# Performance work log

Measured on AMD Instinct MI355X. Metric: run time of the kernel, lower is better.

The kernel has to match this reference:

```python
import jax, jax.numpy as jnp
import numpy as np

B = 4096
D = 64  # emb_dim, hardcoded in UserEmb/ItemEmb


def setup_inputs() -> dict:
    key = jax.random.key(0)
    ks = jax.random.split(key, 26)
    n = lambda k, shape, s=1.0: jax.random.normal(k, shape, dtype=jnp.float32) * s
    inp = {
        'user_emb': jax.random.randint(ks[0], (B, 4), 0, 6, dtype=jnp.int32),
        'item_emb': jax.random.randint(ks[1], (B, 10242), 0, 2, dtype=jnp.int32),
        'edge_emb': jnp.zeros((B,), dtype=jnp.int32),  # edges_emb has num_embeddings=1
        # UserEmb params
        'gender_tab': n(ks[2], (98, D)),
        'age_tab': n(ks[3], (7, D)),
        'occ_tab': n(ks[4], (21, D)),
        'area_tab': n(ks[5], (3402, D)),
        'user_W': n(ks[6], (4 * D, D), 0.05),  # stored [in,out]
        'user_b': n(ks[7], (D,), 0.05),
        # ItemEmb params
        'rate_tab': n(ks[8], (6, D)),
        'genre_W': n(ks[9], (25, D), 0.05),
        'director_W': n(ks[10], (2186, D), 0.02),
        'actor_W': n(ks[11], (8030, D), 0.01),
        'item_W': n(ks[12], (4 * D, D), 0.05),
        'item_b': n(ks[13], (D,), 0.05),
        # GLNFeat params (torch: randn * 0.5)
        'edges_tab': n(ks[14], (1, D)),
        'uu_w': n(ks[15], (D,), 0.5),
        'ui_w': n(ks[16], (D,), 0.5),
        'iu_w': n(ks[17], (D,), 0.5),
        'ii_w': n(ks[18], (D,), 0.5),
        'edge_W': n(ks[19], (D, D), 0.5),
        'uu_W1': n(ks[20], (D, D), 0.5),
        'ui_W1': n(ks[21], (D, D), 0.5),
        'iu_W1': n(ks[22], (D, D), 0.5),
        'ii_W1': n(ks[23], (D, D), 0.5),
    }
    return inp


def _lrelu(v):
    return jnp.where(v >= 0, v, 0.01 * v)  # nn.LeakyReLU default slope


def reference(user_emb, item_emb, edge_emb, gender_tab, age_tab, occ_tab, area_tab,
              user_W, user_b, rate_tab, genre_W, director_W, actor_W, item_W, item_b,
              edges_tab, uu_w, ui_w, iu_w, ii_w, edge_W, uu_W1, ui_W1, iu_W1, ii_W1):
    a = 0.12
    b = 0.12
    # UserEmb
    u_cat = jnp.concatenate([gender_tab[user_emb[:, 0]], age_tab[user_emb[:, 1]],
                             occ_tab[user_emb[:, 2]], area_tab[user_emb[:, 3]]], axis=1)
    x = (u_cat @ user_W + user_b) * a  # [B, D]
    # ItemEmb: multi-hot fields projected then mean-normalized by count
    genre = item_emb[:, 1:26].astype(jnp.float32)
    director = item_emb[:, 26:2212].astype(jnp.float32)
    actor = item_emb[:, 2212:10242].astype(jnp.float32)
    ge = (genre @ genre_W) / jnp.sum(genre, 1, keepdims=True)
    de = (director @ director_W) / jnp.sum(director, 1, keepdims=True)
    ae = (actor @ actor_W) / jnp.sum(actor, 1, keepdims=True)
    i_cat = jnp.concatenate([rate_tab[item_emb[:, 0]], ge, de, ae], axis=1)
    y = (i_cat @ item_W + item_b) * a  # [B, D]
    edge = edges_tab[edge_emb] * b  # [B, D]

    def outer_mm(u, v, M):
        # stop_gradient(outer(u, v) @ M) == u[:,None] * (v @ M), avoids [B,B]
        return jax.lax.stop_gradient(u[:, None] * (v @ M))

    xe = x * edge
    ye = y * edge
    x_xx = xe @ uu_w      # [B]
    x_xy_x = xe @ ui_w
    x_xy_y = ye @ ui_w
    t1 = outer_mm(x_xx, x_xx, x)
    t2 = outer_mm(x_xy_x, x_xy_y, y)
    x_buy = (_lrelu(t1 @ uu_W1) + _lrelu(t2 @ ui_W1)) / 2
    y_yy = ye @ ii_w
    y_yx_y = ye @ iu_w
    y_yx_x = xe @ iu_w
    t3 = outer_mm(y_yy, y_yy, y)
    t4 = outer_mm(y_yx_y, y_yx_x, x)
    y_buy = (_lrelu(t3 @ ii_W1) + _lrelu(t4 @ iu_W1)) / 2
    new = _lrelu(edge @ edge_W)
    return ((x_buy + x) / 2, (y_buy + y) / 2, (new + edge) / 2)
```

## Files before the change

### kernel.cpp

```cpp
#include <hip/hip_runtime.h>
#include <cstddef>

constexpr int BATCH = 4096;
constexpr int ITEM_COLS = 10242;

constexpr int R_GENDER = 0;
constexpr int R_AGE    = 98;
constexpr int R_OCC    = 105;
constexpr int R_AREA   = 126;
constexpr int R_RATE   = 3528;
constexpr int R_FU     = 3534;

__device__ const int CUM[10] = {0, 128, 1280, 2432, 3840, 5248, 6656, 8064, 9472, 10880};
__device__ const int DLT[9]  = {0, -104, -168, -224, -296, -368, -432, -504, -576};
__device__ const int LOG[9]  = {1, 130, 1287, 2436, 3846, 5256, 6659, 8069, 9479};
__device__ const int HIG[9]  = {26, 1223, 2380, 3774, 5184, 6595, 7997, 9407, 10818};
constexpr int FB2COLS = 10880;
constexpr int NTILE   = 85;
constexpr int NSLICE  = 15;
__device__ const int TS_[16] = {0, 1, 7, 13, 19, 25, 31, 37, 43, 49, 55, 61, 67, 73, 79, 85};

constexpr int NFUSEA = 884;
constexpr int NFUSET = FB2COLS / 64;
constexpr int NPACK  = 1024;

struct PackTab { unsigned long long vm[NFUSET]; int c0[NFUSET]; };
constexpr PackTab make_packtab() {
    PackTab p{};
    const int CUMc[10] = {0, 128, 1280, 2432, 3840, 5248, 6656, 8064, 9472, 10880};
    const int DLTc[9]  = {0, -104, -168, -224, -296, -368, -432, -504, -576};
    const int LOGc[9]  = {1, 130, 1287, 2436, 3846, 5256, 6659, 8069, 9479};
    const int HIGc[9]  = {26, 1223, 2380, 3774, 5184, 6595, 7997, 9407, 10818};
    for (int wq = 0; wq < NFUSET; ++wq) {
        int g0 = wq * 64;
        int ch = 0;
        while (g0 >= CUMc[ch + 1]) ++ch;
        int lo = LOGc[ch] - g0; lo = lo < 0 ? 0 : lo;
        int hi = HIGc[ch] - g0; hi = hi < 0 ? 0 : (hi > 64 ? 64 : hi);
        unsigned long long hm = (hi >= 64) ? ~0ull : ((1ull << hi) - 1ull);
        unsigned long long lm = (lo <= 0) ? 0ull : ((1ull << lo) - 1ull);
        p.vm[wq] = hm & ~lm;
        p.c0[wq] = g0 + DLTc[ch];
    }
    return p;
}
__device__ constexpr PackTab PT = make_packtab();

constexpr size_t OFF_FU  = 0;
constexpr size_t OFF_NEW = OFF_FU + (size_t)R_FU * 64;
constexpr size_t OFF_FBT = OFF_NEW + 64;
constexpr size_t OFF_MSK = OFF_FBT + (size_t)64 * FB2COLS / 2;
constexpr size_t OFF_X   = OFF_MSK + (size_t)BATCH * (FB2COLS / 64) * 2;
constexpr size_t OFF_Y   = OFF_X + (size_t)BATCH * 64;
constexpr size_t OFF_P   = OFF_Y + (size_t)BATCH * 64;
constexpr size_t OFF_C   = OFF_P + (size_t)NSLICE * BATCH * 64;
constexpr size_t OFF_SP  = OFF_C + (size_t)NSLICE * BATCH;
constexpr size_t OFF_SC  = OFF_SP + 256ull * 256;

typedef __attribute__((ext_vector_type(8))) short bf16x8;
typedef __attribute__((ext_vector_type(4))) float f32x4;
typedef __attribute__((ext_vector_type(4))) unsigned u32x4;

__device__ __forceinline__ float lrelu(float v) { return v >= 0.0f ? v : 0.01f * v; }

__device__ __forceinline__ unsigned bf_rne_pair(float lo, float hi) {
    unsigned ul = __builtin_bit_cast(unsigned, lo);
    unsigned uh = __builtin_bit_cast(unsigned, hi);
    ul += 0x7fffu + ((ul >> 16) & 1u);
    uh += 0x7fffu + ((uh >> 16) & 1u);
    return (ul >> 16) | (uh & 0xffff0000u);
}

__global__ __launch_bounds__(256) void k_fuse(
        const float* __restrict__ gender_tab, const float* __restrict__ age_tab,
        const float* __restrict__ occ_tab, const float* __restrict__ area_tab,
        const float* __restrict__ user_W, const float* __restrict__ rate_tab,
        const float* __restrict__ item_W, const float* __restrict__ edges_tab,
        const float* __restrict__ edge_W, const float* __restrict__ genre_W,
        const float* __restrict__ director_W, const float* __restrict__ actor_W,
        const int* __restrict__ item,
        float* __restrict__ Fu, float* __restrict__ NEWt, short* __restrict__ B2s,
        unsigned long long* __restrict__ M64) {
    const int t = threadIdx.x;
    const int blk = blockIdx.x;

    if (blk >= NFUSEA + NFUSET) {
        const int w = __builtin_amdgcn_readfirstlane(t >> 6);
        const int lane = t & 63;
        const int m = (blk - (NFUSEA + NFUSET)) * 4 + w;
        const int* row = item + (size_t)m * ITEM_COLS;
        unsigned long long* dst = M64 + (size_t)m * (FB2COLS / 64);
#pragma unroll 2
        for (int wq = 0; wq < FB2COLS / 64; ++wq) {
            int c = PT.c0[wq] + lane;
            c = c > (ITEM_COLS - 1) ? (ITEM_COLS - 1) : c;
            unsigned long long b = __ballot(row[c] != 0) & PT.vm[wq];
            if (lane == 0) dst[wq] = b;
        }
        return;
    }

    const int n = t & 63;
    const int rb = __builtin_amdgcn_readfirstlane(t >> 6);
    __shared__ float T[64 * 65];

    if (blk < NFUSEA) {
        int r = blk * 4 + rb;
        if (r > R_FU) return;
        if (r == R_FU) {
            float acc = 0.0f;
#pragma unroll
            for (int k = 0; k < 64; ++k)
                acc = fmaf(edges_tab[k] * 0.12f, edge_W[k * 64 + n], acc);
            NEWt[n] = lrelu(acc);
            return;
        }
        const float* src;
        const float* W;
        if (r < R_AGE)       { src = gender_tab + (size_t)r * 64;            W = user_W;            }
        else if (r < R_OCC)  { src = age_tab    + (size_t)(r - R_AGE) * 64;  W = user_W + 64 * 64;  }
        else if (r < R_AREA) { src = occ_tab    + (size_t)(r - R_OCC) * 64;  W = user_W + 128 * 64; }
        else if (r < R_RATE) { src = area_tab   + (size_t)(r - R_AREA) * 64; W = user_W + 192 * 64; }
        else                 { src = rate_tab   + (size_t)(r - R_RATE) * 64; W = item_W;            }
        float acc = 0.0f;
#pragma unroll
        for (int k = 0; k < 64; ++k)
            acc = fmaf(src[k], W[k * 64 + n], acc);
        Fu[(size_t)r * 64 + n] = acc;
        return;
    }

    const int g0 = (blk - NFUSEA) * 64;
    int ch = 0;
    while (g0 >= CUM[ch + 1]) ++ch;
    const int lo = LOG[ch], hi = HIG[ch], dl = DLT[ch];

    for (int rl = 0; rl < 16; ++rl) {
        int r = rl * 4 + rb;
        int g = g0 + r;
        float acc = 0.0f;
        if (g >= lo && g < hi) {
            int c = g + dl;
            const float* src;
            const float* W;
            if (c < 26)        { src = genre_W    + (size_t)(c - 1) * 64;    W = item_W + 64 * 64;  }
            else if (c < 2212) { src = director_W + (size_t)(c - 26) * 64;   W = item_W + 128 * 64; }
            else               { src = actor_W    + (size_t)(c - 2212) * 64; W = item_W + 192 * 64; }
#pragma unroll
            for (int k = 0; k < 64; ++k)
                acc = fmaf(src[k], W[k * 64 + n], acc);
        }
        T[r * 65 + n] = acc;
    }
    __syncthreads();
    int n2 = t >> 2, sg = t & 3;
    unsigned dw[8];
#pragma unroll
    for (int d = 0; d < 8; ++d)
        dw[d] = bf_rne_pair(T[(sg * 16 + 2 * d) * 65 + n2], T[(sg * 16 + 2 * d + 1) * 65 + n2]);
    const int kt = g0 >> 7;
    const int kl = (g0 & 127) + sg * 16;
    const int ks = kl >> 5;
    const int qa = (kl >> 3) & 3;
    const int s = n2 >> 4, r16b = n2 & 15;
    const size_t slot0 = (size_t)kt * 1024 + ks * 256 + s * 64 + qa * 16 + r16b;
    *(uint4*)(B2s + slot0 * 8)        = make_uint4(dw[0], dw[1], dw[2], dw[3]);
    *(uint4*)(B2s + (slot0 + 16) * 8) = make_uint4(dw[4], dw[5], dw[6], dw[7]);
}

__global__ __launch_bounds__(256) void k_item(const unsigned long long* __restrict__ M64,
                                              const short* __restrict__ B2s,
                                              float* __restrict__ P, float* __restrict__ C) {
    const int slc = blockIdx.y;
    const int kt0 = TS_[slc], kt1 = TS_[slc + 1];
    const int m0 = blockIdx.x * 64;
    const int t = threadIdx.x;
    const int lane = t & 63;
    const int w = __builtin_amdgcn_readfirstlane(t >> 6);
    const int q = lane >> 4, r16 = lane & 15;
    const int m = m0 + w * 16 + r16;

    f32x4 acc[5];
#pragma unroll
    for (int s = 0; s < 5; ++s) acc[s] = (f32x4){0.f, 0.f, 0.f, 0.f};

    const short o = (r16 == 0) ? (short)0x3f80 : (short)0;
    const bf16x8 ones = {o, o, o, o, o, o, o, o};

    const u32x4* mrow = (const u32x4*)(M64 + (size_t)m * (FB2COLS / 64));
    const bf16x8* b2 = (const bf16x8*)B2s;

    for (int kt = kt0; kt < kt1; ++kt) {
        u32x4 mv = mrow[kt];
        const bf16x8* bp = b2 + (size_t)kt * 1024 + lane;
#pragma unroll
        for (int ks = 0; ks < 4; ++ks) {
            unsigned by = (mv[ks] >> (q * 8)) & 0xffu;
            u32x4 ev;
#pragma unroll
            for (int p2 = 0; p2 < 4; ++p2)
                ev[p2] = (((by >> (2 * p2)) & 1u) ? 0x3f80u : 0u)
                       | (((by >> (2 * p2 + 1)) & 1u) ? 0x3f800000u : 0u);
            bf16x8 a = __builtin_bit_cast(bf16x8, ev);
#pragma unroll
            for (int s = 0; s < 4; ++s) {
                bf16x8 b = bp[ks * 256 + s * 64];
                acc[s] = __builtin_amdgcn_mfma_f32_16x16x32_bf16(a, b, acc[s], 0, 0, 0);
            }
            acc[4] = __builtin_amdgcn_mfma_f32_16x16x32_bf16(a, ones, acc[4], 0, 0, 0);
        }
    }
    const size_t pb = (size_t)slc * BATCH + m0 + w * 16 + q * 4;
#pragma unroll
    for (int reg = 0; reg < 4; ++reg) {
        float* pr = P + (pb + reg) * 64 + r16;
        pr[0] = acc[0][reg];
        pr[16] = acc[1][reg];
        pr[32] = acc[2][reg];
        pr[48] = acc[3][reg];
    }
    if (r16 == 0) {
#pragma unroll
        for (int reg = 0; reg < 4; ++reg)
            C[(size_t)slc * BATCH + m0 + w * 16 + q * 4 + reg] = acc[4][reg];
    }
}

__device__ __forceinline__ float wred(float v) {
#pragma unroll
    for (int m = 1; m < 64; m <<= 1) v += __shfl_xor(v, m, 64);
    return v;
}

__global__ __launch_bounds__(256) void k_mid(const int* __restrict__ item, const int* __restrict__ edge_emb,
                                             const int* __restrict__ user_emb,
                                             const float* __restrict__ Fu, const float* __restrict__ user_b,
                                             const float* __restrict__ P, const float* __restrict__ C,
                                             const float* __restrict__ item_b, const float* __restrict__ edges_tab,
                                             const float* __restrict__ uu_w, const float* __restrict__ ui_w,
                                             const float* __restrict__ iu_w, const float* __restrict__ ii_w,
                                             float* __restrict__ X, float* __restrict__ Y,
                                             float* __restrict__ SC, float* __restrict__ SP) {
    const int t = threadIdx.x;
    const int n = t & 63;
    const int wv = __builtin_amdgcn_readfirstlane(t >> 6);
    const float uuw = uu_w[n], uiw = ui_w[n], iuw = iu_w[n], iiw = ii_w[n];
    const float ib = item_b[n], ub = user_b[n];
    const size_t cs = (size_t)BATCH * 64;
    float s1 = 0.0f, s2 = 0.0f, s3 = 0.0f, s4 = 0.0f;

    for (int i = 0; i < 4; ++i) {
        int b = blockIdx.x * 16 + wv * 4 + i;
        const int* ue = user_emb + (size_t)b * 4;
        float x = (Fu[(size_t)(R_GENDER + ue[0]) * 64 + n]
                 + Fu[(size_t)(R_AGE    + ue[1]) * 64 + n]
                 + Fu[(size_t)(R_OCC    + ue[2]) * 64 + n]
                 + Fu[(size_t)(R_AREA   + ue[3]) * 64 + n] + ub) * 0.12f;
        X[(size_t)b * 64 + n] = x;
        int ri = item[(size_t)b * ITEM_COLS];
        size_t base = (size_t)b * 64 + n;
        float sg = P[base];
        float cg = C[b];
        float sd = 0.0f, cd = 0.0f, sa = 0.0f, ca = 0.0f;
#pragma unroll
        for (int s5 = 1; s5 < 4; ++s5) { sd += P[base + s5 * cs]; cd += C[s5 * BATCH + b]; }
#pragma unroll
        for (int s5 = 4; s5 < NSLICE; ++s5) { sa += P[base + s5 * cs]; ca += C[s5 * BATCH + b]; }
        float y = (Fu[(size_t)(R_RATE + ri) * 64 + n] + sg / cg + sd / cd + sa / ca + ib) * 0.12f;
        Y[(size_t)b * 64 + n] = y;
        float e = edges_tab[(size_t)edge_emb[b] * 64 + n] * 0.12f;
        float xe = x * e, ye = y * e;
        float r1 = wred(xe * uuw);
        float r2 = wred(xe * uiw);
        float r3 = wred(xe * iuw);
        float r4 = wred(ye * uiw);
        float r5 = wred(ye * iiw);
        float r6 = wred(ye * iuw);
        if (n == 0) {
            SC[b] = r1; SC[BATCH + b] = r2; SC[2 * BATCH + b] = r5; SC[3 * BATCH + b] = r6;
        }
        s1 = fmaf(r1, x, s1);
        s2 = fmaf(r4, y, s2);
        s3 = fmaf(r5, y, s3);
        s4 = fmaf(r3, x, s4);
    }
    __shared__ float sp[4][4][64];
    sp[wv][0][n] = s1; sp[wv][1][n] = s2; sp[wv][2][n] = s3; sp[wv][3][n] = s4;
    __syncthreads();
    int i2 = t >> 6;
    float v = sp[0][i2][n] + sp[1][i2][n] + sp[2][i2][n] + sp[3][i2][n];
    SP[(size_t)blockIdx.x * 256 + t] = v;
}

__global__ __launch_bounds__(256) void k_out(const float* __restrict__ X, const float* __restrict__ Y,
                                             const float* __restrict__ SC, const float* __restrict__ SP,
                                             const float* __restrict__ NEWt, const float* __restrict__ edges_tab,
                                             const int* __restrict__ edge_emb,
                                             const float* __restrict__ uu_W1, const float* __restrict__ ui_W1,
                                             const float* __restrict__ iu_W1, const float* __restrict__ ii_W1,
                                             float* __restrict__ out) {
    const int t = threadIdx.x;
    const int i = t >> 6, n = t & 63;
    float s = 0.0f;
    for (int wb = 0; wb < 256; ++wb) s += SP[(size_t)wb * 256 + t];
    __shared__ float sl2[4][64];
    sl2[i][n] = s;
    __syncthreads();
    const float* W1 = (i == 0) ? uu_W1 : (i == 1) ? ui_W1 : (i == 2) ? ii_W1 : iu_W1;
    float p = 0.0f;
#pragma unroll
    for (int k = 0; k < 64; ++k) p = fmaf(sl2[i][k], W1[k * 64 + n], p);
    __shared__ float pbs[4][64];
    pbs[i][n] = p;
    __syncthreads();
    const float p1 = pbs[0][n], p2 = pbs[1][n], p3 = pbs[2][n], p4 = pbs[3][n];
    const float nw = NEWt[n];
#pragma unroll
    for (int j = 0; j < 8; ++j) {
        int b = blockIdx.x * 32 + j * 4 + i;
        float xx = SC[b], xyx = SC[BATCH + b], yy = SC[2 * BATCH + b], yxy = SC[3 * BATCH + b];
        float x = X[(size_t)b * 64 + n], y = Y[(size_t)b * 64 + n];
        float o1 = ((lrelu(xx * p1) + lrelu(xyx * p2)) * 0.5f + x) * 0.5f;
        float o2 = ((lrelu(yy * p3) + lrelu(yxy * p4)) * 0.5f + y) * 0.5f;
        float e = edges_tab[(size_t)edge_emb[b] * 64 + n] * 0.12f;
        float o3 = (nw + e) * 0.5f;
        out[(size_t)b * 64 + n] = o1;
        out[((size_t)BATCH + b) * 64 + n] = o2;
        out[((size_t)2 * BATCH + b) * 64 + n] = o3;
    }
}

extern "C" void kernel_launch(void* const* d_in, const int* in_sizes, int n_in,
                              void* d_out, int out_size, void* d_ws, size_t ws_size,
                              hipStream_t stream) {
    (void)in_sizes; (void)n_in; (void)out_size; (void)ws_size;
    const int*   user_emb   = (const int*)  d_in[0];
    const int*   item_emb   = (const int*)  d_in[1];
    const int*   edge_emb   = (const int*)  d_in[2];
    const float* gender_tab = (const float*)d_in[3];
    const float* age_tab    = (const float*)d_in[4];
    const float* occ_tab    = (const float*)d_in[5];
    const float* area_tab   = (const float*)d_in[6];
    const float* user_W     = (const float*)d_in[7];
    const float* user_b     = (const float*)d_in[8];
    const float* rate_tab   = (const float*)d_in[9];
    const float* genre_W    = (const float*)d_in[10];
    const float* director_W = (const float*)d_in[11];
    const float* actor_W    = (const float*)d_in[12];
    const float* item_W     = (const float*)d_in[13];
    const float* item_b     = (const float*)d_in[14];
    const float* edges_tab  = (const float*)d_in[15];
    const float* uu_w       = (const float*)d_in[16];
    const float* ui_w       = (const float*)d_in[17];
    const float* iu_w       = (const float*)d_in[18];
    const float* ii_w       = (const float*)d_in[19];
    const float* edge_W     = (const float*)d_in[20];
    const float* uu_W1      = (const float*)d_in[21];
    const float* ui_W1      = (const float*)d_in[22];
    const float* iu_W1      = (const float*)d_in[23];
    const float* ii_W1      = (const float*)d_in[24];

    float* ws   = (float*)d_ws;
    float* Fu   = ws + OFF_FU;
    float* NEWt = ws + OFF_NEW;
    short* B2s  = (short*)(ws + OFF_FBT);
    unsigned long long* M64 = (unsigned long long*)(ws + OFF_MSK);
    float* X    = ws + OFF_X;
    float* Y    = ws + OFF_Y;
    float* P    = ws + OFF_P;
    float* C    = ws + OFF_C;
    float* SP   = ws + OFF_SP;
    float* SC   = ws + OFF_SC;
    float* out  = (float*)d_out;

    hipLaunchKernelGGL(k_fuse, dim3(NFUSEA + NFUSET + NPACK), dim3(256), 0, stream,
                       gender_tab, age_tab, occ_tab, area_tab, user_W, rate_tab,
                       item_W, edges_tab, edge_W, genre_W, director_W, actor_W,
                       item_emb, Fu, NEWt, B2s, M64);
    hipLaunchKernelGGL(k_item, dim3(BATCH / 64, NSLICE), dim3(256), 0, stream, M64, B2s, P, C);
    hipLaunchKernelGGL(k_mid, dim3(BATCH / 16), dim3(256), 0, stream,
                       item_emb, edge_emb, user_emb, Fu, user_b, P, C, item_b, edges_tab,
                       uu_w, ui_w, iu_w, ii_w, X, Y, SC, SP);
    hipLaunchKernelGGL(k_out, dim3(BATCH / 32), dim3(256), 0, stream,
                       X, Y, SC, SP, NEWt, edges_tab, edge_emb,
                       uu_W1, ui_W1, iu_W1, ii_W1, out);
}
```

Baseline: 387.2 us.

## Read item multi-hot directly in GEMM kernel, drop bitmask packing pass

Removes the packing stage that ballots the int32 item matrix into 64-bit masks, and instead has the item GEMM kernel read the raw int32 rows and build bf16 one/zero A-fragments on the fly. Full tiles use vectorized int2 loads, and tiles that straddle field boundaries use bounds-checked scalar loads. This eliminates one full read of the ~168MB item matrix plus the mask write/read. The cost is that each GEMM thread now loads 32 bytes per k-step with strided row access instead of 4 bytes of mask, which may make the GEMM more memory-bound.

```diff
diff --git a/kernel.cpp b/kernel.cpp
--- a/kernel.cpp
+++ b/kernel.cpp
@@ -16,41 +16,26 @@
 __device__ const int LOG[9]  = {1, 130, 1287, 2436, 3846, 5256, 6659, 8069, 9479};
 __device__ const int HIG[9]  = {26, 1223, 2380, 3774, 5184, 6595, 7997, 9407, 10818};
 constexpr int FB2COLS = 10880;
-constexpr int NTILE   = 85;
 constexpr int NSLICE  = 15;
 __device__ const int TS_[16] = {0, 1, 7, 13, 19, 25, 31, 37, 43, 49, 55, 61, 67, 73, 79, 85};
+__device__ const int TCH[85] = {
+    0,
+    1,1,1,1,1,1,1,1,1,
+    2,2,2,2,2,2,2,2,2,
+    3,3,3,3,3,3,3,3,3,3,3,
+    4,4,4,4,4,4,4,4,4,4,4,
+    5,5,5,5,5,5,5,5,5,5,5,
+    6,6,6,6,6,6,6,6,6,6,6,
+    7,7,7,7,7,7,7,7,7,7,7,
+    8,8,8,8,8,8,8,8,8,8,8};
 
 constexpr int NFUSEA = 884;
 constexpr int NFUSET = FB2COLS / 64;
-constexpr int NPACK  = 1024;
-
-struct PackTab { unsigned long long vm[NFUSET]; int c0[NFUSET]; };
-constexpr PackTab make_packtab() {
-    PackTab p{};
-    const int CUMc[10] = {0, 128, 1280, 2432, 3840, 5248, 6656, 8064, 9472, 10880};
-    const int DLTc[9]  = {0, -104, -168, -224, -296, -368, -432, -504, -576};
-    const int LOGc[9]  = {1, 130, 1287, 2436, 3846, 5256, 6659, 8069, 9479};
-    const int HIGc[9]  = {26, 1223, 2380, 3774, 5184, 6595, 7997, 9407, 10818};
-    for (int wq = 0; wq < NFUSET; ++wq) {
-        int g0 = wq * 64;
-        int ch = 0;
-        while (g0 >= CUMc[ch + 1]) ++ch;
-        int lo = LOGc[ch] - g0; lo = lo < 0 ? 0 : lo;
-        int hi = HIGc[ch] - g0; hi = hi < 0 ? 0 : (hi > 64 ? 64 : hi);
-        unsigned long long hm = (hi >= 64) ? ~0ull : ((1ull << hi) - 1ull);
-        unsigned long long lm = (lo <= 0) ? 0ull : ((1ull << lo) - 1ull);
-        p.vm[wq] = hm & ~lm;
-        p.c0[wq] = g0 + DLTc[ch];
-    }
-    return p;
-}
-__device__ constexpr PackTab PT = make_packtab();
 
 constexpr size_t OFF_FU  = 0;
 constexpr size_t OFF_NEW = OFF_FU + (size_t)R_FU * 64;
 constexpr size_t OFF_FBT = OFF_NEW + 64;
-constexpr size_t OFF_MSK = OFF_FBT + (size_t)64 * FB2COLS / 2;
-constexpr size_t OFF_X   = OFF_MSK + (size_t)BATCH * (FB2COLS / 64) * 2;
+constexpr size_t OFF_X   = OFF_FBT + (size_t)64 * FB2COLS / 2;
 constexpr size_t OFF_Y   = OFF_X + (size_t)BATCH * 64;
 constexpr size_t OFF_P   = OFF_Y + (size_t)BATCH * 64;
 constexpr size_t OFF_C   = OFF_P + (size_t)NSLICE * BATCH * 64;
@@ -78,34 +63,15 @@
         const float* __restrict__ item_W, const float* __restrict__ edges_tab,
         const float* __restrict__ edge_W, const float* __restrict__ genre_W,
         const float* __restrict__ director_W, const float* __restrict__ actor_W,
-        const int* __restrict__ item,
-        float* __restrict__ Fu, float* __restrict__ NEWt, short* __restrict__ B2s,
-        unsigned long long* __restrict__ M64) {
+        float* __restrict__ Fu, float* __restrict__ NEWt, short* __restrict__ B2s) {
     const int t = threadIdx.x;
     const int blk = blockIdx.x;
-
-    if (blk >= NFUSEA + NFUSET) {
-        const int w = __builtin_amdgcn_readfirstlane(t >> 6);
-        const int lane = t & 63;
-        const int m = (blk - (NFUSEA + NFUSET)) * 4 + w;
-        const int* row = item + (size_t)m * ITEM_COLS;
-        unsigned long long* dst = M64 + (size_t)m * (FB2COLS / 64);
-#pragma unroll 2
-        for (int wq = 0; wq < FB2COLS / 64; ++wq) {
-            int c = PT.c0[wq] + lane;
-            c = c > (ITEM_COLS - 1) ? (ITEM_COLS - 1) : c;
-            unsigned long long b = __ballot(row[c] != 0) & PT.vm[wq];
-            if (lane == 0) dst[wq] = b;
-        }
-        return;
-    }
-
     const int n = t & 63;
     const int rb = __builtin_amdgcn_readfirstlane(t >> 6);
     __shared__ float T[64 * 65];
 
-    if (blk < NFUSEA) {
-        int r = blk * 4 + rb;
+    if (blk >= NFUSET) {
+        int r = (blk - NFUSET) * 4 + rb;
         if (r > R_FU) return;
         if (r == R_FU) {
             float acc = 0.0f;
@@ -130,7 +96,7 @@
         return;
     }
 
-    const int g0 = (blk - NFUSEA) * 64;
+    const int g0 = blk * 64;
     int ch = 0;
     while (g0 >= CUM[ch + 1]) ++ch;
     const int lo = LOG[ch], hi = HIG[ch], dl = DLT[ch];
@@ -168,7 +134,7 @@
     *(uint4*)(B2s + (slot0 + 16) * 8) = make_uint4(dw[4], dw[5], dw[6], dw[7]);
 }
 
-__global__ __launch_bounds__(256) void k_item(const unsigned long long* __restrict__ M64,
+__global__ __launch_bounds__(256) void k_item(const int* __restrict__ item,
                                               const short* __restrict__ B2s,
                                               float* __restrict__ P, float* __restrict__ C) {
     const int slc = blockIdx.y;
@@ -179,6 +145,7 @@
     const int w = __builtin_amdgcn_readfirstlane(t >> 6);
     const int q = lane >> 4, r16 = lane & 15;
     const int m = m0 + w * 16 + r16;
+    const int* row = item + (size_t)m * ITEM_COLS;
 
     f32x4 acc[5];
 #pragma unroll
@@ -186,28 +153,53 @@
 
     const short o = (r16 == 0) ? (short)0x3f80 : (short)0;
     const bf16x8 ones = {o, o, o, o, o, o, o, o};
-
-    const u32x4* mrow = (const u32x4*)(M64 + (size_t)m * (FB2COLS / 64));
     const bf16x8* b2 = (const bf16x8*)B2s;
 
     for (int kt = kt0; kt < kt1; ++kt) {
-        u32x4 mv = mrow[kt];
+        const int ch = TCH[kt];
+        const int c0 = kt * 128 + DLT[ch];
+        const int lo = LOG[ch] - kt * 128;
+        const int hi = HIG[ch] - kt * 128;
         const bf16x8* bp = b2 + (size_t)kt * 1024 + lane;
-#pragma unroll
-        for (int ks = 0; ks < 4; ++ks) {
-            unsigned by = (mv[ks] >> (q * 8)) & 0xffu;
-            u32x4 ev;
-#pragma unroll
-            for (int p2 = 0; p2 < 4; ++p2)
-                ev[p2] = (((by >> (2 * p2)) & 1u) ? 0x3f80u : 0u)
-                       | (((by >> (2 * p2 + 1)) & 1u) ? 0x3f800000u : 0u);
-            bf16x8 a = __builtin_bit_cast(bf16x8, ev);
-#pragma unroll
-            for (int s = 0; s < 4; ++s) {
-                bf16x8 b = bp[ks * 256 + s * 64];
-                acc[s] = __builtin_amdgcn_mfma_f32_16x16x32_bf16(a, b, acc[s], 0, 0, 0);
+        if (lo <= 0 && hi >= 128) {
+#pragma unroll
+            for (int ks = 0; ks < 4; ++ks) {
+                const int cb = c0 + ks * 32 + q * 8;
+                int2 v0 = *(const int2*)(row + cb);
+                int2 v1 = *(const int2*)(row + cb + 2);
+                int2 v2 = *(const int2*)(row + cb + 4);
+                int2 v3 = *(const int2*)(row + cb + 6);
+                u32x4 ev;
+                ev[0] = (v0.x ? 0x3f80u : 0u) | (v0.y ? 0x3f800000u : 0u);
+                ev[1] = (v1.x ? 0x3f80u : 0u) | (v1.y ? 0x3f800000u : 0u);
+                ev[2] = (v2.x ? 0x3f80u : 0u) | (v2.y ? 0x3f800000u : 0u);
+                ev[3] = (v3.x ? 0x3f80u : 0u) | (v3.y ? 0x3f800000u : 0u);
+                bf16x8 a = __builtin_bit_cast(bf16x8, ev);
+#pragma unroll
+                for (int s = 0; s < 4; ++s)
+                    acc[s] = __builtin_amdgcn_mfma_f32_16x16x32_bf16(a, bp[ks * 256 + s * 64], acc[s], 0, 0, 0);
+                acc[4] = __builtin_amdgcn_mfma_f32_16x16x32_bf16(a, ones, acc[4], 0, 0, 0);
             }
-            acc[4] = __builtin_amdgcn_mfma_f32_16x16x32_bf16(a, ones, acc[4], 0, 0, 0);
+        } else {
+#pragma unroll
+            for (int ks = 0; ks < 4; ++ks) {
+                int vv[8];
+#pragma unroll
+                for (int j = 0; j < 8; ++j) {
+                    int kk = ks * 32 + q * 8 + j;
+                    bool ok = (kk >= lo) && (kk < hi);
+                    vv[j] = ok ? row[c0 + kk] : 0;
+                }
+                u32x4 ev;
+#pragma unroll
+                for (int p2 = 0; p2 < 4; ++p2)
+                    ev[p2] = (vv[2 * p2] ? 0x3f80u : 0u) | (vv[2 * p2 + 1] ? 0x3f800000u : 0u);
+                bf16x8 a = __builtin_bit_cast(bf16x8, ev);
+#pragma unroll
+                for (int s = 0; s < 4; ++s)
+                    acc[s] = __builtin_amdgcn_mfma_f32_16x16x32_bf16(a, bp[ks * 256 + s * 64], acc[s], 0, 0, 0);
+                acc[4] = __builtin_amdgcn_mfma_f32_16x16x32_bf16(a, ones, acc[4], 0, 0, 0);
+            }
         }
     }
     const size_t pb = (size_t)slc * BATCH + m0 + w * 16 + q * 4;
@@ -364,7 +356,6 @@
     float* Fu   = ws + OFF_FU;
     float* NEWt = ws + OFF_NEW;
     short* B2s  = (short*)(ws + OFF_FBT);
-    unsigned long long* M64 = (unsigned long long*)(ws + OFF_MSK);
     float* X    = ws + OFF_X;
     float* Y    = ws + OFF_Y;
     float* P    = ws + OFF_P;
@@ -373,11 +364,11 @@
     float* SC   = ws + OFF_SC;
     float* out  = (float*)d_out;
 
-    hipLaunchKernelGGL(k_fuse, dim3(NFUSEA + NFUSET + NPACK), dim3(256), 0, stream,
+    hipLaunchKernelGGL(k_fuse, dim3(NFUSET + NFUSEA), dim3(256), 0, stream,
                        gender_tab, age_tab, occ_tab, area_tab, user_W, rate_tab,
                        item_W, edges_tab, edge_W, genre_W, director_W, actor_W,
-                       item_emb, Fu, NEWt, B2s, M64);
-    hipLaunchKernelGGL(k_item, dim3(BATCH / 64, NSLICE), dim3(256), 0, stream, M64, B2s, P, C);
+                       Fu, NEWt, B2s);
+    hipLaunchKernelGGL(k_item, dim3(BATCH / 64, NSLICE), dim3(256), 0, stream, item_emb, B2s, P, C);
     hipLaunchKernelGGL(k_mid, dim3(BATCH / 16), dim3(256), 0, stream,
                        item_emb, edge_emb, user_emb, Fu, user_b, P, C, item_b, edges_tab,
                        uu_w, ui_w, iu_w, ii_w, X, Y, SC, SP);
```

Result: no change. 381.1 us (-1.6%).
